# Kernel tuning notes

Measured on AMD Instinct MI355X. Metric: run time of the kernel, lower is better.

The kernel has to match this reference:

```python
import jax, jax.numpy as jnp
import numpy as np

GROUP_SIZES = [2048, 4096, 8192, 16384]
TOP_K = 64
L1_COEFF = 1e-3
AUX_PENALTY = 1e-2
N_BATCHES_TO_DEAD = 20
AUX_K_MULT = 16


def setup_inputs() -> dict:
    D = 1024
    S = sum(GROUP_SIZES)  # 30720
    B = 2048
    key = jax.random.key(0)
    k1, k2, k3 = jax.random.split(key, 3)
    x = jax.random.normal(k1, (B, D), dtype=jnp.float32)
    # kaiming_uniform-like init for W_enc [D, S]
    bound = np.sqrt(6.0 / D)
    W_enc = jax.random.uniform(k2, (D, S), jnp.float32, -bound, bound)
    # W_dec = W_enc.T row-normalized (as in __init__)
    W_dec = W_enc.T
    W_dec = W_dec / jnp.linalg.norm(W_dec, axis=-1, keepdims=True)
    b_dec = jnp.zeros((D,), jnp.float32)
    b_enc = jnp.zeros((S,), jnp.float32)
    num_batches_not_active = jax.random.randint(k3, (S,), 0, 40, dtype=jnp.int32)
    return dict(x=x, b_dec=b_dec, b_enc=b_enc, W_enc=W_enc, W_dec=W_dec,
                num_batches_not_active=num_batches_not_active)


def reference(x, b_dec, b_enc, W_enc, W_dec, num_batches_not_active):
    B, D = x.shape
    S = W_enc.shape[1]
    # encoder
    acts = jax.nn.relu((x - b_dec) @ W_enc + b_enc)  # [B, S]
    # global (batch-level) top-k over flattened activations + scatter back
    k = TOP_K * B
    flat = acts.reshape(-1)
    vals, idx = jax.lax.top_k(flat, k)
    acts_topk = jnp.zeros_like(flat).at[idx].set(vals).reshape(B, S)
    # hierarchical group-wise decode with per-group L2 losses
    bounds = np.concatenate([[0], np.cumsum(GROUP_SIZES)]).astype(int)
    recon = jnp.broadcast_to(b_dec, (B, D))
    l2_losses = []
    for i in range(len(GROUP_SIZES)):
        s, e = int(bounds[i]), int(bounds[i + 1])
        recon = recon + acts_topk[:, s:e] @ W_dec[s:e, :]
        l2_losses.append(jnp.mean((recon - x) ** 2))
    mean_l2_loss = jnp.mean(jnp.stack(l2_losses))
    l1_loss = L1_COEFF * jnp.mean(jnp.sum(jnp.abs(acts_topk), axis=-1))
    # auxiliary dead-feature loss
    dead = num_batches_not_active >= N_BATCHES_TO_DEAD  # [S] bool
    residual = jax.lax.stop_gradient(x - recon)
    k_aux = TOP_K * AUX_K_MULT * B  # assumes num_dead * B >= k_aux (holds here)
    masked = jnp.where(dead[None, :], acts, -jnp.inf)
    min_top_k_val = jax.lax.top_k(masked.reshape(-1), k_aux)[0][-1]
    min_top_k_val = jnp.where(jnp.isfinite(min_top_k_val), min_top_k_val, 0.0)
    acts_aux = jax.nn.relu(acts - min_top_k_val) * dead[None, :].astype(acts.dtype)
    recon_aux = acts_aux @ W_dec  # dead-only contribution (others zeroed)
    aux_loss = AUX_PENALTY * jnp.mean((recon_aux - residual) ** 2)
    aux_loss = jnp.where(jnp.any(dead), aux_loss, 0.0)
    total_loss = mean_l2_loss + l1_loss + aux_loss
    l0_norm = jnp.mean(jnp.sum((acts_topk > 0).astype(jnp.float32), axis=-1))
    return total_loss, mean_l2_loss, l1_loss, aux_loss, l0_norm, acts_topk, recon
```

## Files before the change

kernel.cpp:

```cpp
#include <hip/hip_runtime.h>

#define NB 2048
#define ND 1024
#define NS 30720
#define K_MAIN 131072LL
#define K_AUX  2097152LL
#define BAND_CAP 16384
#define SEL_CAP  8192
#define CANDA_CAP 65536
#define EPS_BAND 1e-3f
#define KSPLIT 4

#define OFF_SCAL 0
#define OFF_ACC  256
#define OFF_H1M  512
#define OFF_H1A  16896
#define OFF_H2M  33280
#define OFF_H2A  49664
#define OFF_ZERO_END 66048
#define OFF_DEAD 66048
#define OFF_SEL_IDX 98304
#define OFF_SEL_BITS 131072
#define OFF_BANDI 163840
#define OFF_BANDV 229376
#define OFF_CAB  360448
#define OFF_RAUX 1048576ULL
#define OFF_AH   (OFF_RAUX + (unsigned long long)KSPLIT * NB * ND * 4)
#define OFF_AL   (OFF_AH + 2048ULL*1024*2)
#define OFF_WHT  (OFF_AL + 2048ULL*1024*2)
#define OFF_WLT  (OFF_WHT + 30720ULL*1024*2)
#define WS_NEED_ENC (OFF_WLT + 30720ULL*1024*2)
#define OFF_AXB  OFF_AH
#define OFF_WDT  (OFF_AXB + 2048ULL*30720*2)
#define WS_NEED_AUX (OFF_WDT + 1024ULL*30720*2)

#define S_NDEAD 0
#define S_B1M 1
#define S_REM1M 2
#define S_B1A 3
#define S_REM1A 4
#define S_T24M 5
#define S_BLO 6
#define S_BHI 7
#define S_T24A 8
#define S_JA 9
#define S_NHI 10
#define S_BANDC 11
#define S_CCA 12
#define S_SELCNT 13
#define S_L0 14
#define S_MINBITS 15

#define A_L2_0 0
#define A_L1 4
#define A_AUX 5

typedef __attribute__((ext_vector_type(8))) short bf16x8;
typedef __attribute__((ext_vector_type(4))) float f32x4;

__device__ __forceinline__ float blk_reduce(float v, float* sred) {
    int t = threadIdx.x;
    #pragma unroll
    for (int o = 32; o > 0; o >>= 1) v += __shfl_down(v, o, 64);
    __syncthreads();
    if ((t & 63) == 0) sred[t >> 6] = v;
    __syncthreads();
    return sred[0] + sred[1] + sred[2] + sred[3];
}

__device__ __forceinline__ unsigned short f2bf(float f) {
    unsigned u = __float_as_uint(f);
    unsigned r = (u + 0x7FFFu + ((u >> 16) & 1u)) >> 16;
    return (unsigned short)r;
}
__device__ __forceinline__ float bf2f(unsigned short h) {
    return __uint_as_float(((unsigned)h) << 16);
}

#define GLD16(gp, lp) __builtin_amdgcn_global_load_lds( \
    (const __attribute__((address_space(1))) unsigned int*)(gp), \
    (__attribute__((address_space(3))) unsigned int*)(lp), 16, 0, 0)

__global__ void k_init(int* w) {
    int n = OFF_ZERO_END / 4;
    for (int i = blockIdx.x * blockDim.x + threadIdx.x; i < n; i += gridDim.x * blockDim.x)
        w[i] = 0;
}

__global__ void k_dead(const int* __restrict__ nbna, unsigned char* __restrict__ dead, int* scal) {
    int stride = gridDim.x * blockDim.x;
    int cnt = 0;
    for (int i = blockIdx.x * blockDim.x + threadIdx.x; i < NS; i += stride) {
        bool d = nbna[i] >= 20;
        dead[i] = d ? 1 : 0;
        cnt += d ? 1 : 0;
    }
    #pragma unroll
    for (int o = 32; o > 0; o >>= 1) cnt += __shfl_down(cnt, o, 64);
    if ((threadIdx.x & 63) == 0 && cnt) atomicAdd(&scal[S_NDEAD], cnt);
}

__global__ void k_prep_a(const float* __restrict__ x, const float* __restrict__ b_dec,
                         unsigned short* __restrict__ Ahg, unsigned short* __restrict__ Alg) {
    int stride = gridDim.x * blockDim.x;
    for (int i = blockIdx.x * blockDim.x + threadIdx.x; i < NB * ND; i += stride) {
        float v = x[i] - b_dec[i & (ND - 1)];
        unsigned short h = f2bf(v);
        unsigned short l = f2bf(v - bf2f(h));
        Ahg[i] = h; Alg[i] = l;
    }
}

__global__ __launch_bounds__(256) void k_prep_w(const float* __restrict__ W,
        unsigned short* __restrict__ WhT, unsigned short* __restrict__ WlT) {
    __shared__ float tile[32][33];
    int n0 = blockIdx.x * 32, k0 = blockIdx.y * 32;
    int t = threadIdx.x;
    int c = t & 31, r = t >> 5;
    #pragma unroll
    for (int it = 0; it < 4; it++)
        tile[r + it * 8][c] = W[(size_t)(k0 + r + it * 8) * NS + n0 + c];
    __syncthreads();
    int kl = t & 31, nl = t >> 5;
    #pragma unroll
    for (int it = 0; it < 4; it++) {
        float v = tile[kl][nl + it * 8];
        unsigned short h = f2bf(v);
        unsigned short l = f2bf(v - bf2f(h));
        size_t o = (size_t)(n0 + nl + it * 8) * ND + k0 + kl;
        WhT[o] = h; WlT[o] = l;
    }
}

#define ENC_STAGE(bufoff, p, gptr, r, ktn) GLD16((gptr) + (size_t)(r) * 128 * ND + (size_t)(ktn) * 32, \
    smem + (bufoff) + (p) * 8192 + (r) * 4096 + ldsw)

#define ENC_RD_AH(boff) { _Pragma("unroll") \
    for (int i = 0; i < 8; i++) ah[i] = *(const bf16x8*)&smem[(boff) + (arb + i * 16) * 32 + cph8]; }
#define ENC_RD_AL(boff) { _Pragma("unroll") \
    for (int i = 0; i < 8; i++) al[i] = *(const bf16x8*)&smem[(boff) + 8192 + (arb + i * 16) * 32 + cph8]; }
#define ENC_RD_BH(boff) { _Pragma("unroll") \
    for (int j = 0; j < 4; j++) bh[j] = *(const bf16x8*)&smem[(boff) + 2 * 8192 + (brb + j * 16) * 32 + cph8]; }
#define ENC_RD_BL(boff) { _Pragma("unroll") \
    for (int j = 0; j < 4; j++) bl[j] = *(const bf16x8*)&smem[(boff) + 3 * 8192 + (brb + j * 16) * 32 + cph8]; }

#define ENC_MFMA(AF, BF) { \
    asm volatile("s_waitcnt lgkmcnt(0)" ::: "memory"); \
    __builtin_amdgcn_sched_barrier(0); \
    __builtin_amdgcn_s_setprio(1); \
    _Pragma("unroll") for (int i = 0; i < 8; i++) \
        _Pragma("unroll") for (int j = 0; j < 4; j++) \
            acc[i][j] = __builtin_amdgcn_mfma_f32_16x16x32_bf16(AF[i], BF[j], acc[i][j], 0, 0, 0); \
    __builtin_amdgcn_s_setprio(0); }

__global__ __launch_bounds__(512, 2) void k_enc_mfma(
        const unsigned short* __restrict__ Ahg, const unsigned short* __restrict__ Alg,
        const unsigned short* __restrict__ WhT, const unsigned short* __restrict__ WlT,
        const float* __restrict__ b_enc, const unsigned char* __restrict__ dead,
        float* __restrict__ acts, int* __restrict__ h1m, int* __restrict__ h1a) {
    __shared__ unsigned short smem[65536];
    const int t = threadIdx.x;
    const int lane = t & 63, w = t >> 6;
    const int wm = w >> 2, wn = w & 3;
    const int flat = blockIdx.x;
    const int wg = (flat & 7) * 120 + (flat >> 3);
    const int n0 = (wg >> 3) * 256;
    const int m0 = (wg & 7) * 256;
    const int ln15 = lane & 15, q = lane >> 4;
    const int cph8 = ((q ^ ((lane >> 1) & 3)) << 3);

    const int srow = w * 16 + (lane >> 2);
    const int sq8 = (((lane & 3) ^ ((lane >> 3) & 3)) << 3);
    const unsigned short* gA  = Ahg + (size_t)(m0 + srow) * ND + sq8;
    const unsigned short* gAl = Alg + (size_t)(m0 + srow) * ND + sq8;
    const unsigned short* gB  = WhT + (size_t)(n0 + srow) * ND + sq8;
    const unsigned short* gBl = WlT + (size_t)(n0 + srow) * ND + sq8;
    const int ldsw = w * 512;

    f32x4 acc[8][4];
    #pragma unroll
    for (int i = 0; i < 8; i++)
        #pragma unroll
        for (int j = 0; j < 4; j++) acc[i][j] = (f32x4){0.f, 0.f, 0.f, 0.f};

    const int arb = wm * 128 + ln15;
    const int brb = wn * 64 + ln15;

    ENC_STAGE(0, 0, gA, 0, 0);  ENC_STAGE(0, 0, gA, 1, 0);
    ENC_STAGE(0, 2, gB, 0, 0);  ENC_STAGE(0, 2, gB, 1, 0);
    ENC_STAGE(0, 3, gBl, 0, 0); ENC_STAGE(0, 3, gBl, 1, 0);
    ENC_STAGE(0, 1, gAl, 0, 0); ENC_STAGE(0, 1, gAl, 1, 0);

    for (int kt = 0; kt < 31; ++kt) {
        const int cboff = (kt & 1) * 32768;
        const int nboff = cboff ^ 32768;
        const int kn = kt + 1;
        bf16x8 ah[8], bh[4], bl[4], al[8];

        ENC_STAGE(nboff, 0, gA, 0, kn);  ENC_STAGE(nboff, 0, gA, 1, kn);
        ENC_STAGE(nboff, 2, gB, 0, kn);  ENC_STAGE(nboff, 2, gB, 1, kn);
        asm volatile("s_waitcnt vmcnt(8)" ::: "memory");
        __builtin_amdgcn_s_barrier();
        ENC_RD_AH(cboff) ENC_RD_BH(cboff)
        ENC_MFMA(ah, bh)

        ENC_STAGE(nboff, 3, gBl, 0, kn); ENC_STAGE(nboff, 3, gBl, 1, kn);
        ENC_STAGE(nboff, 1, gAl, 0, kn); ENC_STAGE(nboff, 1, gAl, 1, kn);
        asm volatile("s_waitcnt vmcnt(8)" ::: "memory");
        __builtin_amdgcn_s_barrier();
        ENC_RD_BL(cboff)
        ENC_MFMA(ah, bl)

        ENC_RD_AL(cboff)
        ENC_MFMA(al, bh)
    }

    {
        const int cboff = 32768;
        bf16x8 ah[8], bh[4], bl[4], al[8];
        asm volatile("s_waitcnt vmcnt(4)" ::: "memory");
        __builtin_amdgcn_s_barrier();
        ENC_RD_AH(cboff) ENC_RD_BH(cboff)
        ENC_MFMA(ah, bh)
        asm volatile("s_waitcnt vmcnt(0)" ::: "memory");
        __builtin_amdgcn_s_barrier();
        ENC_RD_BL(cboff)
        ENC_MFMA(ah, bl)
        ENC_RD_AL(cboff)
        ENC_MFMA(al, bh)
    }

    __syncthreads();
    int* hh = (int*)smem;
    for (int i2 = t; i2 < 16384; i2 += 512) hh[i2] = 0;
    __syncthreads();

    const int ln3 = lane & 3;
    int zc = 0, zca = 0;
    #pragma unroll
    for (int j = 0; j < 4; j++) {
        int n = n0 + wn * 64 + j * 16 + ln15;
        float be = b_enc[n];
        int dd = dead[n] ? 1 : 0;
        #pragma unroll
        for (int i = 0; i < 8; i++) {
            int mrow = m0 + wm * 128 + i * 16 + q * 4;
            #pragma unroll
            for (int rg = 0; rg < 4; rg++) {
                float v = fmaxf(acc[i][j][rg] + be, 0.f);
                acts[(size_t)(mrow + rg) * NS + n] = v;
                unsigned bits = __float_as_uint(v);
                if (bits == 0u) { zc++; zca += dd; }
                else atomicAdd(&hh[((bits >> 20) << 2) | ln3], 1 + (dd << 16));
            }
        }
    }
    #pragma unroll
    for (int o = 32; o > 0; o >>= 1) { zc += __shfl_down(zc, o, 64); zca += __shfl_down(zca, o, 64); }
    if ((t & 63) == 0 && (zc | zca)) atomicAdd(&hh[w & 3], zc + (zca << 16));
    __syncthreads();
    for (int b2 = t; b2 < 4096; b2 += 512) {
        unsigned w0 = (unsigned)hh[b2 * 4 + 0], w1 = (unsigned)hh[b2 * 4 + 1];
        unsigned w2 = (unsigned)hh[b2 * 4 + 2], w3 = (unsigned)hh[b2 * 4 + 3];
        int m = (int)((w0 & 0xFFFFu) + (w1 & 0xFFFFu) + (w2 & 0xFFFFu) + (w3 & 0xFFFFu));
        int a = (int)((w0 >> 16) + (w1 >> 16) + (w2 >> 16) + (w3 >> 16));
        if (m) atomicAdd(&h1m[b2], m);
        if (a) atomicAdd(&h1a[b2], a);
    }
}

#define GBM 128
#define GBN 128
#define GBK 8
__global__ __launch_bounds__(256) void k_enc_gemm(const float* __restrict__ x,
        const float* __restrict__ b_dec, const float* __restrict__ b_enc,
        const float* __restrict__ W, float* __restrict__ acts) {
    __shared__ float As[GBK][GBM];
    __shared__ float Bs[GBK][GBN];
    const int t = threadIdx.x;
    const int tx = t & 15, ty = t >> 4;
    const int m0 = blockIdx.y * GBM, n0 = blockIdx.x * GBN;
    const int am = t >> 1, ak = (t & 1) * 4;
    const int bk = t >> 5, bnq = (t & 31) * 4;
    float acc[8][8];
    #pragma unroll
    for (int i = 0; i < 8; i++)
        #pragma unroll
        for (int j = 0; j < 8; j++) acc[i][j] = 0.f;
    for (int k0 = 0; k0 < ND; k0 += GBK) {
        float4 av = *(const float4*)(x + (size_t)(m0 + am) * ND + k0 + ak);
        float4 bd = *(const float4*)(b_dec + k0 + ak);
        As[ak + 0][am] = av.x - bd.x;
        As[ak + 1][am] = av.y - bd.y;
        As[ak + 2][am] = av.z - bd.z;
        As[ak + 3][am] = av.w - bd.w;
        *(float4*)&Bs[bk][bnq] = *(const float4*)(W + (size_t)(k0 + bk) * NS + n0 + bnq);
        __syncthreads();
        #pragma unroll
        for (int kk = 0; kk < GBK; kk++) {
            float a[8], b[8];
            *(float4*)&a[0] = *(const float4*)&As[kk][ty * 4];
            *(float4*)&a[4] = *(const float4*)&As[kk][64 + ty * 4];
            *(float4*)&b[0] = *(const float4*)&Bs[kk][tx * 4];
            *(float4*)&b[4] = *(const float4*)&Bs[kk][64 + tx * 4];
            #pragma unroll
            for (int i = 0; i < 8; i++)
                #pragma unroll
                for (int j = 0; j < 8; j++)
                    acc[i][j] = fmaf(a[i], b[j], acc[i][j]);
        }
        __syncthreads();
    }
    float be[8];
    #pragma unroll
    for (int j = 0; j < 4; j++) {
        be[j]     = b_enc[n0 + tx * 4 + j];
        be[4 + j] = b_enc[n0 + 64 + tx * 4 + j];
    }
    #pragma unroll
    for (int i = 0; i < 8; i++) {
        int row = m0 + ((i < 4) ? (ty * 4 + i) : (64 + ty * 4 + i - 4));
        float* orow = acts + (size_t)row * NS + n0;
        #pragma unroll
        for (int j = 0; j < 4; j++) {
            orow[tx * 4 + j]      = fmaxf(acc[i][j] + be[j], 0.f);
            orow[64 + tx * 4 + j] = fmaxf(acc[i][4 + j] + be[4 + j], 0.f);
        }
    }
}

__global__ __launch_bounds__(256) void k_hist1(const float* __restrict__ acts,
        const unsigned char* __restrict__ dead, int* h1m, int* h1a) {
    __shared__ int hm[4096], ha[4096];
    int t = threadIdx.x;
    for (int i = t; i < 4096; i += 256) { hm[i] = 0; ha[i] = 0; }
    __syncthreads();
    for (int row = blockIdx.x; row < NB; row += gridDim.x) {
        const float* pr = acts + (size_t)row * NS;
        for (int c = t; c < NS; c += 256) {
            unsigned bits = __float_as_uint(pr[c]);
            bool isz = (bits == 0u);
            bool dd = dead[c] != 0;
            unsigned long long mz = __ballot(isz);
            unsigned long long mza = __ballot(isz && dd);
            if ((t & 63) == 0) {
                int nz = __popcll(mz);
                if (nz) atomicAdd(&hm[0], nz);
                int nza = __popcll(mza);
                if (nza) atomicAdd(&ha[0], nza);
            }
            if (!isz) {
                atomicAdd(&hm[bits >> 20], 1);
                if (dd) atomicAdd(&ha[bits >> 20], 1);
            }
        }
    }
    __syncthreads();
    for (int i = t; i < 4096; i += 256) {
        if (hm[i]) atomicAdd(&h1m[i], hm[i]);
        if (ha[i]) atomicAdd(&h1a[i], ha[i]);
    }
}

__global__ void k_scan(const int* __restrict__ hist, int* scal, int mode) {
    __shared__ long long csum[256];
    __shared__ long long totsh;
    int t = threadIdx.x;
    int base = t * 16;
    int h[16];
    long long loc = 0;
    #pragma unroll
    for (int i = 0; i < 16; i++) { h[i] = hist[base + i]; loc += h[i]; }
    csum[t] = loc;
    __syncthreads();
    if (t == 0) {
        long long run = 0;
        for (int c = 255; c >= 0; c--) { long long tmp = csum[c]; csum[c] = run; run += tmp; }
        totsh = run;
    }
    __syncthreads();
    long long k;
    if (mode == 0) k = K_MAIN;
    else if (mode == 1) k = K_AUX;
    else if (mode == 2) k = (long long)scal[S_REM1M];
    else {
        if (scal[S_B1A] < 0) { if (t == 0) { scal[S_T24A] = -1; scal[S_MINBITS] = 0; } return; }
        k = (long long)scal[S_REM1A];
    }
    if (mode == 1 && k > totsh) { if (t == 0) scal[S_B1A] = -1; return; }
    long long cum = csum[t];
    int fb = -1; long long rem = 0;
    for (int i = 15; i >= 0; i--) {
        long long ca = cum;
        cum += h[i];
        if (ca < k && k <= cum) { fb = base + i; rem = k - ca; }
    }
    if (fb >= 0) {
        if (mode == 0)      { scal[S_B1M] = fb; scal[S_REM1M] = (int)rem; }
        else if (mode == 1) { scal[S_B1A] = fb; scal[S_REM1A] = (int)rem; }
        else if (mode == 2) {
            int t24 = (scal[S_B1M] << 12) | fb;
            scal[S_T24M] = t24;
            float center = __uint_as_float((((unsigned)t24) << 8) | 128u);
            float lo = center - EPS_BAND;
            if (lo < 0.f) lo = 0.f;
            scal[S_BLO] = (int)__float_as_uint(lo);
            scal[S_BHI] = (int)__float_as_uint(center + EPS_BAND);
        }
        else { scal[S_T24A] = (scal[S_B1A] << 12) | fb; scal[S_JA] = (int)rem; }
    }
}

__global__ __launch_bounds__(256) void k_hist2(const float* __restrict__ acts,
        const unsigned char* __restrict__ dead, const int* scal, int* h2m, int* h2a) {
    int b1m = scal[S_B1M], b1a = scal[S_B1A];
    int row = blockIdx.x, t = threadIdx.x;
    const float* pr = acts + (size_t)row * NS;
    for (int c = t; c < NS; c += 256) {
        unsigned bits = __float_as_uint(pr[c]);
        int hi = (int)(bits >> 20);
        if (hi == b1m) atomicAdd(&h2m[(bits >> 8) & 0xFFF], 1);
        if (b1a >= 0 && hi == b1a && dead[c]) atomicAdd(&h2a[(bits >> 8) & 0xFFF], 1);
    }
}

__global__ __launch_bounds__(256) void k_collect(const float* __restrict__ acts,
        const unsigned char* __restrict__ dead, int* scal,
        int* bandi, unsigned* cab) {
    int row = blockIdx.x, t = threadIdx.x;
    unsigned blo = (unsigned)scal[S_BLO], bhi = (unsigned)scal[S_BHI];
    int t24a = scal[S_T24A];
    const float* pr = acts + (size_t)row * NS;
    int cnt = 0;
    for (int c = t; c < NS; c += 256) {
        unsigned bits = __float_as_uint(pr[c]);
        if (bits > bhi) cnt++;
        else if (bits >= blo) {
            int p = atomicAdd(&scal[S_BANDC], 1);
            if (p < BAND_CAP) bandi[p] = row * NS + c;
        }
        if (t24a >= 0 && (bits >> 8) == (unsigned)t24a && dead[c]) {
            int p = atomicAdd(&scal[S_CCA], 1);
            if (p < CANDA_CAP) cab[p] = bits;
        }
    }
    #pragma unroll
    for (int o = 32; o > 0; o >>= 1) cnt += __shfl_down(cnt, o, 64);
    __shared__ int s2[4];
    if ((t & 63) == 0) s2[t >> 6] = cnt;
    __syncthreads();
    if (t == 0) {
        int tot = s2[0] + s2[1] + s2[2] + s2[3];
        if (tot) atomicAdd(&scal[S_NHI], tot);
    }
}

__global__ __launch_bounds__(256) void k_resolve(const unsigned* __restrict__ cab, int* scal) {
    __shared__ int h[256];
    int t = threadIdx.x;
    h[t] = 0;
    __syncthreads();
    int t24a = scal[S_T24A];
    if (t24a < 0) { if (t == 0) scal[S_MINBITS] = 0; return; }
    int cnt = min(scal[S_CCA], CANDA_CAP);
    int ja = scal[S_JA];
    for (int e = t; e < cnt; e += 256) atomicAdd(&h[cab[e] & 0xFF], 1);
    __syncthreads();
    if (t == 0) {
        long long cum = 0; int L = 0;
        for (int b = 255; b >= 0; b--) {
            long long ca = cum; cum += h[b];
            if (ca < ja && ja <= cum) { L = b; break; }
        }
        scal[S_MINBITS] = (int)((((unsigned)t24a) << 8) | (unsigned)L);
    }
}

__global__ __launch_bounds__(256) void k_band_re(const float* __restrict__ x,
        const float* __restrict__ b_dec, const float* __restrict__ b_enc,
        const float* __restrict__ W, const int* scal,
        const int* __restrict__ bandi, double* __restrict__ bandv) {
    int n = min(scal[S_BANDC], BAND_CAP);
    int t = threadIdx.x;
    __shared__ double sd[4];
    for (int e = blockIdx.x; e < n; e += gridDim.x) {
        int idx = bandi[e];
        int r = idx / NS, c = idx - r * NS;
        double s = 0.0;
        #pragma unroll
        for (int j = 0; j < 4; j++) {
            int d = t + j * 256;
            s += ((double)x[(size_t)r * ND + d] - (double)b_dec[d]) * (double)W[(size_t)d * NS + c];
        }
        #pragma unroll
        for (int o = 32; o > 0; o >>= 1) s += __shfl_down(s, o, 64);
        if ((t & 63) == 0) sd[t >> 6] = s;
        __syncthreads();
        if (t == 0) {
            double v = sd[0] + sd[1] + sd[2] + sd[3] + (double)b_enc[c];
            bandv[e] = fmax(v, 0.0);
        }
        __syncthreads();
    }
}

__global__ __launch_bounds__(256) void k_band_sel(int* scal,
        const int* __restrict__ bandi, const double* __restrict__ bandv,
        int* sel_idx, unsigned* sel_bits) {
    int n = min(scal[S_BANDC], BAND_CAP);
    int need = (int)(K_MAIN - (long long)scal[S_NHI]);
    if (need < 0) need = 0;
    if (need > n) need = n;
    int t = threadIdx.x;
    for (int e = t; e < n; e += 256) {
        double v = bandv[e];
        int idx = bandi[e];
        int rank = 0;
        for (int j = 0; j < n; j++) {
            double vj = bandv[j];
            rank += (vj > v || (vj == v && bandi[j] < idx)) ? 1 : 0;
        }
        if (rank < need) {
            int p = atomicAdd(&scal[S_SELCNT], 1);
            if (p < SEL_CAP) { sel_idx[p] = idx; sel_bits[p] = __float_as_uint((float)v); }
        }
    }
}

__global__ __launch_bounds__(256) void k_decode(float* __restrict__ acts,
        const float* __restrict__ x, const float* __restrict__ b_dec, const float* __restrict__ Wd,
        float* __restrict__ recon, const unsigned char* __restrict__ dead,
        const int* __restrict__ sel_idx, unsigned short* __restrict__ axb,
        int* scal, double* acc, int fuse) {
    int row = blockIdx.x, t = threadIdx.x;
    unsigned blo = (unsigned)scal[S_BLO], bhi = (unsigned)scal[S_BHI];
    float minval = __uint_as_float((unsigned)scal[S_MINBITS]);
    int selcnt = min(scal[S_SELCNT], SEL_CAP);
    __shared__ int lj[2048];
    __shared__ float lv[2048];
    __shared__ int lcnt;
    __shared__ float sred[4];
    const int d0 = t * 4;
    float4 r;
    r.x = b_dec[d0]; r.y = b_dec[d0 + 1]; r.z = b_dec[d0 + 2]; r.w = b_dec[d0 + 3];
    float4 xv = *(const float4*)(x + (size_t)row * ND + d0);
    float* arow = acts + (size_t)row * NS;
    unsigned short* xrow = axb + (size_t)row * NS;
    float l1 = 0.f; int kcnt = 0;
    const int bnds[5] = {0, 2048, 6144, 14336, NS};
    for (int g = 0; g < 4; g++) {
        for (int c0 = bnds[g]; c0 < bnds[g + 1]; c0 += 2048) {
            __syncthreads();
            if (t == 0) lcnt = 0;
            __syncthreads();
            #pragma unroll
            for (int u = 0; u < 8; u++) {
                int c = c0 + u * 256 + t;
                float v = arow[c];
                unsigned bits = __float_as_uint(v);
                bool strict = bits > bhi;
                bool keep = strict;
                if (!keep && bits >= blo) {
                    int flat = row * NS + c;
                    for (int e = 0; e < selcnt; e++)
                        if (sel_idx[e] == flat) { keep = true; break; }
                }
                if (keep) { int p = atomicAdd(&lcnt, 1); lj[p] = c; lv[p] = v; }
                if (fuse) {
                    if (strict) { l1 += v; kcnt++; }
                    arow[c] = strict ? v : 0.f;
                    float o = (dead[c] && v > minval) ? (v - minval) : 0.f;
                    xrow[c] = f2bf(o);
                }
            }
            __syncthreads();
            int n = lcnt;
            for (int e = 0; e < n; e++) {
                float a_ = lv[e];
                float4 w = *(const float4*)(Wd + (size_t)lj[e] * ND + d0);
                r.x = fmaf(a_, w.x, r.x);
                r.y = fmaf(a_, w.y, r.y);
                r.z = fmaf(a_, w.z, r.z);
                r.w = fmaf(a_, w.w, r.w);
            }
        }
        float dx = r.x - xv.x, dy = r.y - xv.y, dz = r.z - xv.z, dw = r.w - xv.w;
        float ss = dx * dx + dy * dy + dz * dz + dw * dw;
        float tot = blk_reduce(ss, sred);
        if (t == 0) atomicAdd(&acc[A_L2_0 + g], (double)tot);
    }
    float* orow = recon + (size_t)row * ND + d0;
    orow[0] = r.x; orow[1] = r.y; orow[2] = r.z; orow[3] = r.w;
    if (fuse) {
        #pragma unroll
        for (int o = 32; o > 0; o >>= 1) { l1 += __shfl_down(l1, o, 64); kcnt += __shfl_down(kcnt, o, 64); }
        __shared__ float s1[4];
        __shared__ int s2[4];
        if ((t & 63) == 0) { s1[t >> 6] = l1; s2[t >> 6] = kcnt; }
        __syncthreads();
        if (t == 0) {
            atomicAdd(&acc[A_L1], (double)(s1[0] + s1[1] + s1[2] + s1[3]));
            atomicAdd(&scal[S_L0], s2[0] + s2[1] + s2[2] + s2[3]);
        }
    }
}

__global__ __launch_bounds__(256) void k_aux_pack(const float* __restrict__ acts,
        const unsigned char* __restrict__ dead, const int* scal,
        unsigned short* __restrict__ axb) {
    int row = blockIdx.x, t = threadIdx.x;
    float minval = __uint_as_float((unsigned)scal[S_MINBITS]);
    const float* arow = acts + (size_t)row * NS;
    unsigned short* orow = axb + (size_t)row * NS;
    for (int c = t; c < NS; c += 256) {
        float v = arow[c];
        float o = (dead[c] && v > minval) ? (v - minval) : 0.f;
        orow[c] = f2bf(o);
    }
}

__global__ __launch_bounds__(256) void k_prep_wd(const float* __restrict__ Wd,
        unsigned short* __restrict__ WdT) {
    __shared__ float tile[32][33];
    int s0 = blockIdx.x * 32, d0 = blockIdx.y * 32;
    int t = threadIdx.x;
    int c = t & 31, r = t >> 5;
    #pragma unroll
    for (int it = 0; it < 4; it++)
        tile[r + it * 8][c] = Wd[(size_t)(s0 + r + it * 8) * ND + d0 + c];
    __syncthreads();
    int sl = t & 31, dl = t >> 5;
    #pragma unroll
    for (int it = 0; it < 4; it++)
        WdT[(size_t)(d0 + dl + it * 8) * NS + s0 + sl] = f2bf(tile[sl][dl + it * 8]);
}

__global__ __launch_bounds__(256) void k_aux_mfma(
        const unsigned short* __restrict__ axb, const unsigned short* __restrict__ WdT,
        float* __restrict__ raux) {
    __shared__ unsigned short smem[16384];
    const int t = threadIdx.x;
    const int lane = t & 63, w = t >> 6;
    const int wm = w >> 1, wn = w & 1;
    const int m0 = blockIdx.y * 128, n0 = blockIdx.x * 128;
    const int kbase = blockIdx.z * (NS / KSPLIT);
    const int ln15 = lane & 15, q = lane >> 4;
    const int cph8 = ((q ^ ((lane >> 1) & 3)) << 3);
    const int sq8 = (((lane & 3) ^ ((lane >> 3) & 3)) << 3);

    f32x4 acc[4][4];
    #pragma unroll
    for (int i = 0; i < 4; i++)
        #pragma unroll
        for (int j = 0; j < 4; j++) acc[i][j] = (f32x4){0.f, 0.f, 0.f, 0.f};

    const unsigned short* gbase;
    int ldst;
    if (w < 2) { gbase = axb + (size_t)(m0 + w * 64) * NS; ldst = w * 64 * 32; }
    else       { gbase = WdT + (size_t)(n0 + (w - 2) * 64) * NS; ldst = 4096 + (w - 2) * 64 * 32; }
    const unsigned short* glane = gbase + (size_t)(lane >> 2) * NS + sq8 + kbase;
    ldst += (lane >> 2) * 32 + (lane & 3) * 8;

    #pragma unroll
    for (int ch = 0; ch < 4; ch++)
        GLD16(glane + (size_t)ch * 16 * NS, smem + ldst + ch * 512);

    const int NKT = (NS / KSPLIT) / 32;
    for (int kt = 0; kt < NKT; ++kt) {
        const int cb = (kt & 1) * 8192;
        const int nb = cb ^ 8192;
        asm volatile("s_waitcnt vmcnt(0)" ::: "memory");
        __builtin_amdgcn_s_barrier();
        __builtin_amdgcn_sched_barrier(0);
        if (kt < NKT - 1) {
            #pragma unroll
            for (int ch = 0; ch < 4; ch++)
                GLD16(glane + (size_t)ch * 16 * NS + (size_t)(kt + 1) * 32, smem + nb + ldst + ch * 512);
        }
        bf16x8 af[4], bf[4];
        #pragma unroll
        for (int i = 0; i < 4; i++)
            af[i] = *(const bf16x8*)&smem[cb + (wm * 64 + i * 16 + ln15) * 32 + cph8];
        #pragma unroll
        for (int j = 0; j < 4; j++)
            bf[j] = *(const bf16x8*)&smem[cb + 4096 + (wn * 64 + j * 16 + ln15) * 32 + cph8];
        asm volatile("s_waitcnt lgkmcnt(0)" ::: "memory");
        __builtin_amdgcn_sched_barrier(0);
        __builtin_amdgcn_s_setprio(1);
        #pragma unroll
        for (int j = 0; j < 4; j++)
            #pragma unroll
            for (int i = 0; i < 4; i++)
                acc[i][j] = __builtin_amdgcn_mfma_f32_16x16x32_bf16(af[i], bf[j], acc[i][j], 0, 0, 0);
        __builtin_amdgcn_s_setprio(0);
    }
    float* rz = raux + (size_t)blockIdx.z * NB * ND;
    #pragma unroll
    for (int j = 0; j < 4; j++) {
        int n = n0 + wn * 64 + j * 16 + ln15;
        #pragma unroll
        for (int i = 0; i < 4; i++) {
            int mrow = m0 + wm * 64 + i * 16 + q * 4;
            #pragma unroll
            for (int rg = 0; rg < 4; rg++)
                rz[(size_t)(mrow + rg) * ND + n] = acc[i][j][rg];
        }
    }
}

__global__ __launch_bounds__(256) void k_aux_diff(const float* __restrict__ raux,
        const float* __restrict__ x, const float* __restrict__ recon, double* acc) {
    __shared__ float sred[4];
    float ss = 0.f;
    int stride = gridDim.x * blockDim.x;
    for (int i = blockIdx.x * blockDim.x + threadIdx.x; i < NB * ND; i += stride) {
        float ra = raux[i];
        #pragma unroll
        for (int z = 1; z < KSPLIT; z++) ra += raux[(size_t)z * NB * ND + i];
        float d = ra - (x[i] - recon[i]);
        ss += d * d;
    }
    float tot = blk_reduce(ss, sred);
    if (threadIdx.x == 0) atomicAdd(&acc[A_AUX], (double)tot);
}

__global__ __launch_bounds__(256) void k_aux(const float* __restrict__ acts,
        const unsigned char* __restrict__ dead, const float* __restrict__ x,
        const float* __restrict__ recon, const float* __restrict__ Wd,
        const int* scal, double* acc) {
    int row = blockIdx.x, t = threadIdx.x;
    float minval = __uint_as_float((unsigned)scal[S_MINBITS]);
    __shared__ int lj[2048];
    __shared__ float lv[2048];
    __shared__ int lcnt;
    __shared__ float sred[4];
    float4 r = {0.f, 0.f, 0.f, 0.f};
    const float* arow = acts + (size_t)row * NS;
    const int d0 = t * 4;
    for (int c0 = 0; c0 < NS; c0 += 2048) {
        __syncthreads();
        if (t == 0) lcnt = 0;
        __syncthreads();
        #pragma unroll
        for (int u = 0; u < 8; u++) {
            int c = c0 + u * 256 + t;
            float v = arow[c];
            if (dead[c] && v > minval) {
                int p = atomicAdd(&lcnt, 1);
                lj[p] = c; lv[p] = v - minval;
            }
        }
        __syncthreads();
        int n = lcnt;
        for (int e = 0; e < n; e++) {
            float a_ = lv[e];
            float4 w = *(const float4*)(Wd + (size_t)lj[e] * ND + d0);
            r.x = fmaf(a_, w.x, r.x);
            r.y = fmaf(a_, w.y, r.y);
            r.z = fmaf(a_, w.z, r.z);
            r.w = fmaf(a_, w.w, r.w);
        }
    }
    const float* xr = x + (size_t)row * ND + d0;
    const float* rr = recon + (size_t)row * ND + d0;
    float dx = r.x - (xr[0] - rr[0]);
    float dy = r.y - (xr[1] - rr[1]);
    float dz = r.z - (xr[2] - rr[2]);
    float dw = r.w - (xr[3] - rr[3]);
    float ss = dx * dx + dy * dy + dz * dz + dw * dw;
    float tot = blk_reduce(ss, sred);
    if (t == 0) atomicAdd(&acc[A_AUX], (double)tot);
}

__global__ __launch_bounds__(256) void k_topk_write(float* __restrict__ out, const int* scal, double* acc, int* scalw) {
    unsigned bhi = (unsigned)scal[S_BHI];
    float l1 = 0.f;
    int cnt = 0;
    const long long vstart = 8, nvec = 15728639;
    long long stride = (long long)gridDim.x * blockDim.x;
    for (long long i = (long long)blockIdx.x * blockDim.x + threadIdx.x; i < nvec; i += stride) {
        float4* p = (float4*)(out + vstart) + i;
        float4 v = *p;
        #define PROC(F) { unsigned b = __float_as_uint(v.F); if (b > bhi) { l1 += v.F; cnt++; } else v.F = 0.f; }
        PROC(x) PROC(y) PROC(z) PROC(w)
        #undef PROC
        *p = v;
    }
    if (blockIdx.x == 0 && threadIdx.x == 0) {
        const long long head[4] = {5, 6, 7, 62914564LL};
        for (int q = 0; q < 4; q++) {
            float v = out[head[q]];
            unsigned b = __float_as_uint(v);
            if (b > bhi) { l1 += v; cnt++; } else out[head[q]] = 0.f;
        }
    }
    int t = threadIdx.x;
    #pragma unroll
    for (int o = 32; o > 0; o >>= 1) { l1 += __shfl_down(l1, o, 64); cnt += __shfl_down(cnt, o, 64); }
    __shared__ float s1[4];
    __shared__ int s2[4];
    if ((t & 63) == 0) { s1[t >> 6] = l1; s2[t >> 6] = cnt; }
    __syncthreads();
    if (t == 0) {
        atomicAdd(&acc[A_L1], (double)(s1[0] + s1[1] + s1[2] + s1[3]));
        atomicAdd(&scalw[S_L0], s2[0] + s2[1] + s2[2] + s2[3]);
    }
}

__global__ __launch_bounds__(256) void k_selwrite(float* __restrict__ acts, const int* __restrict__ sel_idx,
        const unsigned* __restrict__ sel_bits, int* scal, double* acc) {
    int t = threadIdx.x;
    int n = min(scal[S_SELCNT], SEL_CAP);
    float l1 = 0.f;
    for (int e = t; e < n; e += 256) {
        float v = __uint_as_float(sel_bits[e]);
        acts[sel_idx[e]] = v;
        l1 += v;
    }
    #pragma unroll
    for (int o = 32; o > 0; o >>= 1) l1 += __shfl_down(l1, o, 64);
    __shared__ float s1[4];
    if ((t & 63) == 0) s1[t >> 6] = l1;
    __syncthreads();
    if (t == 0) {
        atomicAdd(&acc[A_L1], (double)(s1[0] + s1[1] + s1[2] + s1[3]));
        atomicAdd(&scal[S_L0], n);
    }
}

__global__ void k_final(float* out, const int* scal, const double* acc) {
    if (threadIdx.x == 0 && blockIdx.x == 0) {
        double ml2 = (acc[0] + acc[1] + acc[2] + acc[3]) * 0.25 / ((double)NB * ND);
        double l1 = 1e-3 * acc[A_L1] / (double)NB;
        double aux = (scal[S_NDEAD] > 0) ? (1e-2 * acc[A_AUX] / ((double)NB * ND)) : 0.0;
        out[0] = (float)(ml2 + l1 + aux);
        out[1] = (float)ml2;
        out[2] = (float)l1;
        out[3] = (float)aux;
        out[4] = (float)scal[S_L0] / (float)NB;
    }
}

extern "C" void kernel_launch(void* const* d_in, const int* in_sizes, int n_in,
                              void* d_out, int out_size, void* d_ws, size_t ws_size,
                              hipStream_t stream) {
    const float* x     = (const float*)d_in[0];
    const float* b_dec = (const float*)d_in[1];
    const float* b_enc = (const float*)d_in[2];
    const float* W_enc = (const float*)d_in[3];
    const float* W_dec = (const float*)d_in[4];
    const int*   nbna  = (const int*)d_in[5];

    float* out = (float*)d_out;
    float* acts  = out + 5;
    float* recon = out + 5 + (size_t)NB * NS;

    char* ws = (char*)d_ws;
    int*    scal = (int*)(ws + OFF_SCAL);
    double* acc  = (double*)(ws + OFF_ACC);
    int*    h1m  = (int*)(ws + OFF_H1M);
    int*    h1a  = (int*)(ws + OFF_H1A);
    int*    h2m  = (int*)(ws + OFF_H2M);
    int*    h2a  = (int*)(ws + OFF_H2A);
    unsigned char* dead = (unsigned char*)(ws + OFF_DEAD);
    int*      sel_idx  = (int*)(ws + OFF_SEL_IDX);
    unsigned* sel_bits = (unsigned*)(ws + OFF_SEL_BITS);
    int*      bandi = (int*)(ws + OFF_BANDI);
    double*   bandv = (double*)(ws + OFF_BANDV);
    unsigned* cab   = (unsigned*)(ws + OFF_CAB);
    float*    raux  = (float*)(ws + OFF_RAUX);
    unsigned short* Ahg = (unsigned short*)(ws + OFF_AH);
    unsigned short* Alg = (unsigned short*)(ws + OFF_AL);
    unsigned short* WhT = (unsigned short*)(ws + OFF_WHT);
    unsigned short* WlT = (unsigned short*)(ws + OFF_WLT);
    unsigned short* axb = (unsigned short*)(ws + OFF_AXB);
    unsigned short* WdT = (unsigned short*)(ws + OFF_WDT);

    const bool use_mfma     = (ws_size >= WS_NEED_ENC);
    const bool use_aux_gemm = (ws_size >= WS_NEED_AUX);

    k_init<<<64, 256, 0, stream>>>((int*)d_ws);
    k_dead<<<60, 256, 0, stream>>>(nbna, dead, scal);
    if (use_mfma) {
        k_prep_a<<<512, 256, 0, stream>>>(x, b_dec, Ahg, Alg);
        k_prep_w<<<dim3(NS / 32, ND / 32), 256, 0, stream>>>(W_enc, WhT, WlT);
        k_enc_mfma<<<(NB / 256) * (NS / 256), 512, 0, stream>>>(Ahg, Alg, WhT, WlT, b_enc, dead, acts, h1m, h1a);
    } else {
        k_enc_gemm<<<dim3(NS / GBN, NB / GBM), 256, 0, stream>>>(x, b_dec, b_enc, W_enc, acts);
        k_hist1<<<1024, 256, 0, stream>>>(acts, dead, h1m, h1a);
    }
    k_scan<<<1, 256, 0, stream>>>(h1m, scal, 0);
    k_scan<<<1, 256, 0, stream>>>(h1a, scal, 1);
    k_hist2<<<NB, 256, 0, stream>>>(acts, dead, scal, h2m, h2a);
    k_scan<<<1, 256, 0, stream>>>(h2m, scal, 2);
    k_scan<<<1, 256, 0, stream>>>(h2a, scal, 3);
    k_collect<<<NB, 256, 0, stream>>>(acts, dead, scal, bandi, cab);
    k_resolve<<<1, 256, 0, stream>>>(cab, scal);
    k_band_re<<<512, 256, 0, stream>>>(x, b_dec, b_enc, W_enc, scal, bandi, bandv);
    k_band_sel<<<1, 256, 0, stream>>>(scal, bandi, bandv, sel_idx, sel_bits);
    if (use_aux_gemm) {
        k_decode<<<NB, 256, 0, stream>>>(acts, x, b_dec, W_dec, recon, dead, sel_idx, axb, scal, acc, 1);
        k_prep_wd<<<dim3(NS / 32, ND / 32), 256, 0, stream>>>(W_dec, WdT);
        k_aux_mfma<<<dim3(ND / 128, NB / 128, KSPLIT), 256, 0, stream>>>(axb, WdT, raux);
        k_aux_diff<<<512, 256, 0, stream>>>(raux, x, recon, acc);
    } else {
        k_decode<<<NB, 256, 0, stream>>>(acts, x, b_dec, W_dec, recon, dead, sel_idx, axb, scal, acc, 0);
        k_aux<<<NB, 256, 0, stream>>>(acts, dead, x, recon, W_dec, scal, acc);
        k_topk_write<<<4096, 256, 0, stream>>>(out, scal, acc, scal);
    }
    k_selwrite<<<1, 256, 0, stream>>>(acts, sel_idx, sel_bits, scal, acc);
    k_final<<<1, 64, 0, stream>>>(out, scal, acc);
}
```

Baseline: 1.884 ms.

## Vectorize streaming kernels, use shared histograms and wave-aggregated atomics

Vectorizes the acts, dead and output accesses in the hist2, collect, decode and aux_diff kernels to 4-wide loads and stores. k_hist2 now builds its histograms in shared memory and flushes them to global once per block instead of issuing global atomics per element. k_collect replaces per-element global atomics with ballot-based wave-aggregated atomics. The goal is to cut memory transactions and global atomic contention, at the cost of extra shared memory and ballot overhead per element. The decode kernel also changes its element-to-thread mapping, so the order in which kept entries are appended to the shared list changes.

```diff
diff --git a/kernel.cpp b/kernel.cpp
--- a/kernel.cpp
+++ b/kernel.cpp
@@ -57,6 +57,7 @@
 
 typedef __attribute__((ext_vector_type(8))) short bf16x8;
 typedef __attribute__((ext_vector_type(4))) float f32x4;
+typedef float f32x4u __attribute__((ext_vector_type(4), aligned(4)));
 
 __device__ __forceinline__ float blk_reduce(float v, float* sred) {
     int t = threadIdx.x;
@@ -413,14 +414,30 @@
 
 __global__ __launch_bounds__(256) void k_hist2(const float* __restrict__ acts,
         const unsigned char* __restrict__ dead, const int* scal, int* h2m, int* h2a) {
+    __shared__ int hm[4096], ha[4096];
+    int t = threadIdx.x;
+    for (int i = t; i < 4096; i += 256) { hm[i] = 0; ha[i] = 0; }
+    __syncthreads();
     int b1m = scal[S_B1M], b1a = scal[S_B1A];
-    int row = blockIdx.x, t = threadIdx.x;
+    int row = blockIdx.x;
     const float* pr = acts + (size_t)row * NS;
-    for (int c = t; c < NS; c += 256) {
-        unsigned bits = __float_as_uint(pr[c]);
-        int hi = (int)(bits >> 20);
-        if (hi == b1m) atomicAdd(&h2m[(bits >> 8) & 0xFFF], 1);
-        if (b1a >= 0 && hi == b1a && dead[c]) atomicAdd(&h2a[(bits >> 8) & 0xFFF], 1);
+    for (int c4 = t; c4 < NS / 4; c4 += 256) {
+        int c = c4 * 4;
+        f32x4u v4 = *(const f32x4u*)&pr[c];
+        uchar4 dd4 = *(const uchar4*)(dead + c);
+        unsigned char dda[4] = {dd4.x, dd4.y, dd4.z, dd4.w};
+        #pragma unroll
+        for (int k2 = 0; k2 < 4; k2++) {
+            unsigned bits = __float_as_uint(v4[k2]);
+            int hi = (int)(bits >> 20);
+            if (hi == b1m) atomicAdd(&hm[(bits >> 8) & 0xFFF], 1);
+            if (b1a >= 0 && hi == b1a && dda[k2]) atomicAdd(&ha[(bits >> 8) & 0xFFF], 1);
+        }
+    }
+    __syncthreads();
+    for (int i = t; i < 4096; i += 256) {
+        if (hm[i]) atomicAdd(&h2m[i], hm[i]);
+        if (ha[i]) atomicAdd(&h2a[i], ha[i]);
     }
 }
 
@@ -428,20 +445,47 @@
         const unsigned char* __restrict__ dead, int* scal,
         int* bandi, unsigned* cab) {
     int row = blockIdx.x, t = threadIdx.x;
+    int lane = t & 63;
     unsigned blo = (unsigned)scal[S_BLO], bhi = (unsigned)scal[S_BHI];
     int t24a = scal[S_T24A];
     const float* pr = acts + (size_t)row * NS;
     int cnt = 0;
-    for (int c = t; c < NS; c += 256) {
-        unsigned bits = __float_as_uint(pr[c]);
-        if (bits > bhi) cnt++;
-        else if (bits >= blo) {
-            int p = atomicAdd(&scal[S_BANDC], 1);
-            if (p < BAND_CAP) bandi[p] = row * NS + c;
-        }
-        if (t24a >= 0 && (bits >> 8) == (unsigned)t24a && dead[c]) {
-            int p = atomicAdd(&scal[S_CCA], 1);
-            if (p < CANDA_CAP) cab[p] = bits;
+    for (int c4 = t; c4 < NS / 4; c4 += 256) {
+        int c = c4 * 4;
+        f32x4u v4 = *(const f32x4u*)&pr[c];
+        uchar4 dd4 = *(const uchar4*)(dead + c);
+        unsigned char dda[4] = {dd4.x, dd4.y, dd4.z, dd4.w};
+        #pragma unroll
+        for (int k2 = 0; k2 < 4; k2++) {
+            unsigned bits = __float_as_uint(v4[k2]);
+            bool hi2 = bits > bhi;
+            cnt += hi2 ? 1 : 0;
+            bool band = !hi2 && bits >= blo;
+            unsigned long long mb = __ballot(band);
+            if (mb) {
+                int ldr = __ffsll(mb) - 1;
+                int nb = __popcll(mb);
+                int base = 0;
+                if (lane == ldr) base = atomicAdd(&scal[S_BANDC], nb);
+                base = __shfl(base, ldr, 64);
+                if (band) {
+                    int p = base + __popcll(mb & ((1ull << lane) - 1ull));
+                    if (p < BAND_CAP) bandi[p] = row * NS + c + k2;
+                }
+            }
+            bool ax = (t24a >= 0) && ((bits >> 8) == (unsigned)t24a) && dda[k2];
+            unsigned long long ma = __ballot(ax);
+            if (ma) {
+                int ldr = __ffsll(ma) - 1;
+                int na = __popcll(ma);
+                int base = 0;
+                if (lane == ldr) base = atomicAdd(&scal[S_CCA], na);
+                base = __shfl(base, ldr, 64);
+                if (ax) {
+                    int p = base + __popcll(ma & ((1ull << lane) - 1ull));
+                    if (p < CANDA_CAP) cab[p] = bits;
+                }
+            }
         }
     }
     #pragma unroll
@@ -554,23 +598,33 @@
             if (t == 0) lcnt = 0;
             __syncthreads();
             #pragma unroll
-            for (int u = 0; u < 8; u++) {
-                int c = c0 + u * 256 + t;
-                float v = arow[c];
-                unsigned bits = __float_as_uint(v);
-                bool strict = bits > bhi;
-                bool keep = strict;
-                if (!keep && bits >= blo) {
-                    int flat = row * NS + c;
-                    for (int e = 0; e < selcnt; e++)
-                        if (sel_idx[e] == flat) { keep = true; break; }
+            for (int u = 0; u < 2; u++) {
+                int c = c0 + (u * 256 + t) * 4;
+                f32x4u v4 = *(const f32x4u*)&arow[c];
+                uchar4 dd4 = *(const uchar4*)(dead + c);
+                unsigned char dda[4] = {dd4.x, dd4.y, dd4.z, dd4.w};
+                f32x4u m4;
+                unsigned short ov[4];
+                #pragma unroll
+                for (int k2 = 0; k2 < 4; k2++) {
+                    float v = v4[k2];
+                    unsigned bits = __float_as_uint(v);
+                    bool strict = bits > bhi;
+                    bool keep = strict;
+                    if (!keep && bits >= blo) {
+                        int flat = row * NS + c + k2;
+                        for (int e = 0; e < selcnt; e++)
+                            if (sel_idx[e] == flat) { keep = true; break; }
+                    }
+                    if (keep) { int p = atomicAdd(&lcnt, 1); lj[p] = c + k2; lv[p] = v; }
+                    if (strict) { l1 += v; kcnt++; }
+                    m4[k2] = strict ? v : 0.f;
+                    float o = (dda[k2] && v > minval) ? (v - minval) : 0.f;
+                    ov[k2] = f2bf(o);
                 }
-                if (keep) { int p = atomicAdd(&lcnt, 1); lj[p] = c; lv[p] = v; }
                 if (fuse) {
-                    if (strict) { l1 += v; kcnt++; }
-                    arow[c] = strict ? v : 0.f;
-                    float o = (dead[c] && v > minval) ? (v - minval) : 0.f;
-                    xrow[c] = f2bf(o);
+                    *(f32x4u*)&arow[c] = m4;
+                    *(ushort4*)&xrow[c] = make_ushort4(ov[0], ov[1], ov[2], ov[3]);
                 }
             }
             __syncthreads();
@@ -589,8 +643,11 @@
         float tot = blk_reduce(ss, sred);
         if (t == 0) atomicAdd(&acc[A_L2_0 + g], (double)tot);
     }
-    float* orow = recon + (size_t)row * ND + d0;
-    orow[0] = r.x; orow[1] = r.y; orow[2] = r.z; orow[3] = r.w;
+    {
+        f32x4u rr;
+        rr[0] = r.x; rr[1] = r.y; rr[2] = r.z; rr[3] = r.w;
+        *(f32x4u*)(recon + (size_t)row * ND + d0) = rr;
+    }
     if (fuse) {
         #pragma unroll
         for (int o = 32; o > 0; o >>= 1) { l1 += __shfl_down(l1, o, 64); kcnt += __shfl_down(kcnt, o, 64); }
@@ -713,12 +770,21 @@
     __shared__ float sred[4];
     float ss = 0.f;
     int stride = gridDim.x * blockDim.x;
-    for (int i = blockIdx.x * blockDim.x + threadIdx.x; i < NB * ND; i += stride) {
-        float ra = raux[i];
-        #pragma unroll
-        for (int z = 1; z < KSPLIT; z++) ra += raux[(size_t)z * NB * ND + i];
-        float d = ra - (x[i] - recon[i]);
-        ss += d * d;
+    for (int i4 = blockIdx.x * blockDim.x + threadIdx.x; i4 < NB * ND / 4; i4 += stride) {
+        int i = i4 * 4;
+        float4 ra = *(const float4*)&raux[i];
+        #pragma unroll
+        for (int z = 1; z < KSPLIT; z++) {
+            float4 rz = *(const float4*)&raux[(size_t)z * NB * ND + i];
+            ra.x += rz.x; ra.y += rz.y; ra.z += rz.z; ra.w += rz.w;
+        }
+        float4 xd = *(const float4*)&x[i];
+        f32x4u rc = *(const f32x4u*)&recon[i];
+        float d0 = ra.x - (xd.x - rc[0]);
+        float d1 = ra.y - (xd.y - rc[1]);
+        float d2 = ra.z - (xd.z - rc[2]);
+        float d3 = ra.w - (xd.w - rc[3]);
+        ss += d0 * d0 + d1 * d1 + d2 * d2 + d3 * d3;
     }
     float tot = blk_reduce(ss, sred);
     if (threadIdx.x == 0) atomicAdd(&acc[A_AUX], (double)tot);
```

Measured after the change: 1.677 ms. 1.12x faster.
